# Kernel tuning notes

Hardware: AMD Instinct MI355X
Metric: run time of the kernel (lower is better)

Reference implementation:

```python
import jax, jax.numpy as jnp
import numpy as np

N_NODES = 100000
N_EDGES = 1600000
IN_DIM = 128
OUT_DIM = 64


def setup_inputs() -> dict:
    key = jax.random.key(0)
    k1, k2, k3, k4, k5 = jax.random.split(key, 5)
    X = jax.random.normal(k1, (N_NODES, IN_DIM), dtype=jnp.float32)
    # reset_parameters: uniform(-stdv, stdv), stdv = 1/sqrt(output_dim)
    stdv = 1.0 / np.sqrt(OUT_DIM)
    weights = jax.random.uniform(k2, (IN_DIM, OUT_DIM), dtype=jnp.float32,
                                 minval=-stdv, maxval=stdv)
    attention_w = jax.random.normal(k3, (1, 1), dtype=jnp.float32)
    edge_src = jnp.sort(jax.random.randint(k4, (N_EDGES,), 0, N_NODES, dtype=jnp.int32))
    edge_dst = jax.random.randint(k5, (N_EDGES,), 0, N_NODES, dtype=jnp.int32)
    return {"X": X, "weights": weights, "attention_w": attention_w,
            "edge_src": edge_src, "edge_dst": edge_dst}


def reference(X, weights, attention_w, edge_src, edge_dst):
    # Dense projection: X_prime = X @ W  -> [N, OUT_DIM]
    X_prime = X @ weights
    # forward_ef: per-edge scalar feature = <X_prime[src], X_prime[dst]>  -> [E]
    src_feat = X_prime[edge_src]          # [E, OUT_DIM] irregular gather
    dst_feat = X_prime[edge_dst]          # [E, OUT_DIM] irregular gather
    edge_feature = jnp.einsum('ed,ed->e', src_feat, dst_feat)
    # edge_attentions = edge_feature[:, None] @ attention_w -> [n_heads=1, E]
    att = edge_feature * attention_w[0, 0]            # [E]
    # forward_AGNN: out[i] = sum_{e:(i->j)} att[e] * X_prime[j]
    msgs = att[:, None] * dst_feat                    # [E, OUT_DIM]
    out = jax.ops.segment_sum(msgs, edge_src, num_segments=X.shape[0])
    return out
```

## Files before the change

### kernel.cpp

```cpp
#include <hip/hip_runtime.h>
#include <stdint.h>

#define N_NODES 100000
#define N_EDGES 1600000
#define IN_DIM 128
#define OUT_DIM 64

typedef __bf16 bf16x8 __attribute__((ext_vector_type(8)));
typedef float  f32x4  __attribute__((ext_vector_type(4)));

__device__ __forceinline__ uint16_t f2bf(float f) {
    uint32_t u = __float_as_uint(f);
    return (uint16_t)((u + 0x7fffu + ((u >> 16) & 1u)) >> 16);
}
__device__ __forceinline__ void unpack8(const uint4& v, float* x) {
    x[0] = __uint_as_float(v.x << 16); x[1] = __uint_as_float(v.x & 0xffff0000u);
    x[2] = __uint_as_float(v.y << 16); x[3] = __uint_as_float(v.y & 0xffff0000u);
    x[4] = __uint_as_float(v.z << 16); x[5] = __uint_as_float(v.z & 0xffff0000u);
    x[6] = __uint_as_float(v.w << 16); x[7] = __uint_as_float(v.w & 0xffff0000u);
}

__global__ __launch_bounds__(256) void prep(const int* __restrict__ src,
                                            const float* __restrict__ W,
                                            int* __restrict__ row_ptr,
                                            uint4* __restrict__ Wfrag) {
    const int b = blockIdx.x;
    if (b < N_EDGES / 256) {
        int e = b * 256 + threadIdx.x;
        int s = src[e];
        if (e == 0) {
            for (int i = 0; i <= s; ++i) row_ptr[i] = 0;
        } else {
            int sp = src[e - 1];
            for (int i = sp + 1; i <= s; ++i) row_ptr[i] = e;
        }
        if (e == N_EDGES - 1) {
            for (int i = s + 1; i <= N_NODES; ++i) row_ptr[i] = N_EDGES;
        }
    } else {
        int item = (b - N_EDGES / 256) * 256 + threadIdx.x;
        if (item < 1024) {
            int f = item >> 6, lane = item & 63;
            int ct = f >> 2, ks = f & 3;
            int col = ct * 16 + (lane & 15);
            int kb  = ks * 32 + (lane >> 4) * 8;
            uint32_t u[4];
            #pragma unroll
            for (int j = 0; j < 4; ++j) {
                uint32_t lo = f2bf(W[(kb + 2 * j)     * OUT_DIM + col]);
                uint32_t hi = f2bf(W[(kb + 2 * j + 1) * OUT_DIM + col]);
                u[j] = lo | (hi << 16);
            }
            Wfrag[f * 64 + lane] = make_uint4(u[0], u[1], u[2], u[3]);
        }
    }
}

__global__ __launch_bounds__(256) void gemm_xw(const float* __restrict__ X,
                                               const uint4* __restrict__ Wfrag,
                                               uint16_t* __restrict__ XPb,
                                               int nRows) {
    const int t = threadIdx.x;
    const int lane = t & 63;

    bf16x8 bfr[16];
    #pragma unroll
    for (int f = 0; f < 16; ++f)
        bfr[f] = __builtin_bit_cast(bf16x8, Wfrag[f * 64 + lane]);

    const int rowBase = blockIdx.x * 64 + (t >> 6) * 16;
    const int r  = rowBase + (lane & 15);
    const int kb = (lane >> 4) * 8;
    const bool inb = r < nRows;

    f32x4 acc[4] = {{0,0,0,0},{0,0,0,0},{0,0,0,0},{0,0,0,0}};

    #pragma unroll
    for (int ks = 0; ks < 4; ++ks) {
        float4 x0 = make_float4(0.f,0.f,0.f,0.f), x1 = x0;
        if (inb) {
            const float* p = &X[(size_t)r * IN_DIM + ks * 32 + kb];
            x0 = *(const float4*)&p[0];
            x1 = *(const float4*)&p[4];
        }
        bf16x8 a;
        a[0]=(__bf16)x0.x; a[1]=(__bf16)x0.y; a[2]=(__bf16)x0.z; a[3]=(__bf16)x0.w;
        a[4]=(__bf16)x1.x; a[5]=(__bf16)x1.y; a[6]=(__bf16)x1.z; a[7]=(__bf16)x1.w;
        #pragma unroll
        for (int ct = 0; ct < 4; ++ct)
            acc[ct] = __builtin_amdgcn_mfma_f32_16x16x32_bf16(a, bfr[ct * 4 + ks], acc[ct], 0, 0, 0);
    }

    const int orow = rowBase + (lane >> 4) * 4;
    const int ocol = lane & 15;
    #pragma unroll
    for (int ct = 0; ct < 4; ++ct) {
        #pragma unroll
        for (int rr = 0; rr < 4; ++rr) {
            int gr = orow + rr;
            if (gr < nRows) XPb[(size_t)gr * OUT_DIM + ct * 16 + ocol] = f2bf(acc[ct][rr]);
        }
    }
}

__global__ __launch_bounds__(256) void agnn_edge(const uint16_t* __restrict__ XPb,
                                                 const int* __restrict__ row_ptr,
                                                 const int* __restrict__ dst,
                                                 const float* __restrict__ aw,
                                                 float* __restrict__ out) {
    const int t = threadIdx.x;
    const int lane = t & 63;
    const int node = blockIdx.x * 4 + (t >> 6);
    if (node >= N_NODES) return;
    const int g = lane >> 3, sl = lane & 7;

    const int lo = row_ptr[node];
    const int hi = row_ptr[node + 1];

    float xq[8];
    {
        uint4 q = *(const uint4*)&XPb[(size_t)node * OUT_DIM + sl * 8];
        unpack8(q, xq);
    }
    float acc[8] = {0.f,0.f,0.f,0.f,0.f,0.f,0.f,0.f};

    for (int e0 = lo; e0 < hi; e0 += 16) {
        const int eA = e0 + g, eB = eA + 8;
        uint4 ra = make_uint4(0u,0u,0u,0u), rb = ra;
        if (eA < hi) {
            int d = dst[eA];
            ra = *(const uint4*)&XPb[(size_t)d * OUT_DIM + sl * 8];
        }
        if (eB < hi) {
            int d = dst[eB];
            rb = *(const uint4*)&XPb[(size_t)d * OUT_DIM + sl * 8];
        }
        float xd[8];
        unpack8(ra, xd);
        float p = xq[0] * xd[0];
        #pragma unroll
        for (int j = 1; j < 8; ++j) p = fmaf(xq[j], xd[j], p);
        p += __shfl_xor(p, 1); p += __shfl_xor(p, 2); p += __shfl_xor(p, 4);
        #pragma unroll
        for (int j = 0; j < 8; ++j) acc[j] = fmaf(p, xd[j], acc[j]);

        unpack8(rb, xd);
        float p2 = xq[0] * xd[0];
        #pragma unroll
        for (int j = 1; j < 8; ++j) p2 = fmaf(xq[j], xd[j], p2);
        p2 += __shfl_xor(p2, 1); p2 += __shfl_xor(p2, 2); p2 += __shfl_xor(p2, 4);
        #pragma unroll
        for (int j = 0; j < 8; ++j) acc[j] = fmaf(p2, xd[j], acc[j]);
    }

    #pragma unroll
    for (int m = 8; m <= 32; m <<= 1) {
        #pragma unroll
        for (int j = 0; j < 8; ++j) acc[j] += __shfl_xor(acc[j], m);
    }
    if (g == 0) {
        const float a = aw[0];
        float* o = &out[(size_t)node * OUT_DIM + sl * 8];
        *(float4*)&o[0] = make_float4(acc[0]*a, acc[1]*a, acc[2]*a, acc[3]*a);
        *(float4*)&o[4] = make_float4(acc[4]*a, acc[5]*a, acc[6]*a, acc[7]*a);
    }
}

extern "C" void kernel_launch(void* const* d_in, const int* in_sizes, int n_in,
                              void* d_out, int out_size, void* d_ws, size_t ws_size,
                              hipStream_t stream) {
    const float* X   = (const float*)d_in[0];
    const float* W   = (const float*)d_in[1];
    const float* aw  = (const float*)d_in[2];
    const int*   src = (const int*)d_in[3];
    const int*   dst = (const int*)d_in[4];
    float* out = (float*)d_out;

    uint16_t* XPb     = (uint16_t*)d_ws;
    int*      row_ptr = (int*)((char*)d_ws + (size_t)N_NODES * OUT_DIM * 2);
    uint4*    Wfrag   = (uint4*)((char*)d_ws + 13200016);

    prep<<<N_EDGES / 256 + 4, 256, 0, stream>>>(src, W, row_ptr, Wfrag);
    gemm_xw<<<(N_NODES + 63) / 64, 256, 0, stream>>>(X, Wfrag, XPb, N_NODES);
    agnn_edge<<<N_NODES / 4, 256, 0, stream>>>(XPb, row_ptr, dst, aw, out);
}
```

Baseline: 70.53 us.

## Store projected features as fp16 and use fdot2 with wider gather batches

Switches the intermediate projected-feature buffer from bf16 to fp16 so the per-edge dot product can use packed fdot2 instructions instead of unpacking to fp32 and doing scalar FMAs. The edge loop now processes 32 edges per iteration, issuing all four destination-index loads and then all four row gathers before computing, so more memory requests are in flight. It also adds a min-blocks hint to launch bounds. fp16 has a narrower range than bf16, which risks overflow if projected values grow large, though the test inputs keep them small.

```diff
diff --git a/kernel.cpp b/kernel.cpp
--- a/kernel.cpp
+++ b/kernel.cpp
@@ -6,18 +6,32 @@
 #define IN_DIM 128
 #define OUT_DIM 64
 
-typedef __bf16 bf16x8 __attribute__((ext_vector_type(8)));
-typedef float  f32x4  __attribute__((ext_vector_type(4)));
+typedef __bf16    bf16x8 __attribute__((ext_vector_type(8)));
+typedef float     f32x4  __attribute__((ext_vector_type(4)));
+typedef _Float16  h2     __attribute__((ext_vector_type(2)));
 
 __device__ __forceinline__ uint16_t f2bf(float f) {
     uint32_t u = __float_as_uint(f);
     return (uint16_t)((u + 0x7fffu + ((u >> 16) & 1u)) >> 16);
 }
-__device__ __forceinline__ void unpack8(const uint4& v, float* x) {
-    x[0] = __uint_as_float(v.x << 16); x[1] = __uint_as_float(v.x & 0xffff0000u);
-    x[2] = __uint_as_float(v.y << 16); x[3] = __uint_as_float(v.y & 0xffff0000u);
-    x[4] = __uint_as_float(v.z << 16); x[5] = __uint_as_float(v.z & 0xffff0000u);
-    x[6] = __uint_as_float(v.w << 16); x[7] = __uint_as_float(v.w & 0xffff0000u);
+__device__ __forceinline__ float hdot8(uint4 a, uint4 b, float c) {
+#if __has_builtin(__builtin_amdgcn_fdot2)
+    c = __builtin_amdgcn_fdot2(__builtin_bit_cast(h2, a.x), __builtin_bit_cast(h2, b.x), c, false);
+    c = __builtin_amdgcn_fdot2(__builtin_bit_cast(h2, a.y), __builtin_bit_cast(h2, b.y), c, false);
+    c = __builtin_amdgcn_fdot2(__builtin_bit_cast(h2, a.z), __builtin_bit_cast(h2, b.z), c, false);
+    c = __builtin_amdgcn_fdot2(__builtin_bit_cast(h2, a.w), __builtin_bit_cast(h2, b.w), c, false);
+#else
+    const h2 qa[4] = {__builtin_bit_cast(h2,a.x),__builtin_bit_cast(h2,a.y),
+                      __builtin_bit_cast(h2,a.z),__builtin_bit_cast(h2,a.w)};
+    const h2 qb[4] = {__builtin_bit_cast(h2,b.x),__builtin_bit_cast(h2,b.y),
+                      __builtin_bit_cast(h2,b.z),__builtin_bit_cast(h2,b.w)};
+    #pragma unroll
+    for (int i = 0; i < 4; ++i) {
+        c = fmaf((float)qa[i][0], (float)qb[i][0], c);
+        c = fmaf((float)qa[i][1], (float)qb[i][1], c);
+    }
+#endif
+    return c;
 }
 
 __global__ __launch_bounds__(256) void prep(const int* __restrict__ src,
@@ -58,7 +72,7 @@
 
 __global__ __launch_bounds__(256) void gemm_xw(const float* __restrict__ X,
                                                const uint4* __restrict__ Wfrag,
-                                               uint16_t* __restrict__ XPb,
+                                               _Float16* __restrict__ XPh,
                                                int nRows) {
     const int t = threadIdx.x;
     const int lane = t & 63;
@@ -98,59 +112,60 @@
         #pragma unroll
         for (int rr = 0; rr < 4; ++rr) {
             int gr = orow + rr;
-            if (gr < nRows) XPb[(size_t)gr * OUT_DIM + ct * 16 + ocol] = f2bf(acc[ct][rr]);
-        }
-    }
-}
-
-__global__ __launch_bounds__(256) void agnn_edge(const uint16_t* __restrict__ XPb,
-                                                 const int* __restrict__ row_ptr,
-                                                 const int* __restrict__ dst,
-                                                 const float* __restrict__ aw,
-                                                 float* __restrict__ out) {
+            if (gr < nRows) XPh[(size_t)gr * OUT_DIM + ct * 16 + ocol] = (_Float16)acc[ct][rr];
+        }
+    }
+}
+
+__global__ __launch_bounds__(256, 6) void agnn_edge(const _Float16* __restrict__ XPh,
+                                                    const int* __restrict__ row_ptr,
+                                                    const int* __restrict__ dst,
+                                                    const float* __restrict__ aw,
+                                                    float* __restrict__ out) {
     const int t = threadIdx.x;
     const int lane = t & 63;
     const int node = blockIdx.x * 4 + (t >> 6);
-    if (node >= N_NODES) return;
     const int g = lane >> 3, sl = lane & 7;
 
     const int lo = row_ptr[node];
     const int hi = row_ptr[node + 1];
 
-    float xq[8];
-    {
-        uint4 q = *(const uint4*)&XPb[(size_t)node * OUT_DIM + sl * 8];
-        unpack8(q, xq);
-    }
+    const uint4 q = *(const uint4*)&XPh[(size_t)node * OUT_DIM + sl * 8];
     float acc[8] = {0.f,0.f,0.f,0.f,0.f,0.f,0.f,0.f};
 
-    for (int e0 = lo; e0 < hi; e0 += 16) {
-        const int eA = e0 + g, eB = eA + 8;
-        uint4 ra = make_uint4(0u,0u,0u,0u), rb = ra;
-        if (eA < hi) {
-            int d = dst[eA];
-            ra = *(const uint4*)&XPb[(size_t)d * OUT_DIM + sl * 8];
-        }
-        if (eB < hi) {
-            int d = dst[eB];
-            rb = *(const uint4*)&XPb[(size_t)d * OUT_DIM + sl * 8];
-        }
-        float xd[8];
-        unpack8(ra, xd);
-        float p = xq[0] * xd[0];
-        #pragma unroll
-        for (int j = 1; j < 8; ++j) p = fmaf(xq[j], xd[j], p);
-        p += __shfl_xor(p, 1); p += __shfl_xor(p, 2); p += __shfl_xor(p, 4);
-        #pragma unroll
-        for (int j = 0; j < 8; ++j) acc[j] = fmaf(p, xd[j], acc[j]);
-
-        unpack8(rb, xd);
-        float p2 = xq[0] * xd[0];
-        #pragma unroll
-        for (int j = 1; j < 8; ++j) p2 = fmaf(xq[j], xd[j], p2);
-        p2 += __shfl_xor(p2, 1); p2 += __shfl_xor(p2, 2); p2 += __shfl_xor(p2, 4);
-        #pragma unroll
-        for (int j = 0; j < 8; ++j) acc[j] = fmaf(p2, xd[j], acc[j]);
+    for (int base = lo; base < hi; base += 32) {
+        int dx[4];
+        #pragma unroll
+        for (int c = 0; c < 4; ++c) {
+            int e = base + c * 8 + g;
+            dx[c] = (e < hi) ? dst[e] : -1;
+        }
+        uint4 xd[4];
+        #pragma unroll
+        for (int c = 0; c < 4; ++c) {
+            xd[c] = make_uint4(0u, 0u, 0u, 0u);
+            if (dx[c] >= 0)
+                xd[c] = *(const uint4*)&XPh[(size_t)dx[c] * OUT_DIM + sl * 8];
+        }
+        #pragma unroll
+        for (int c = 0; c < 4; ++c) {
+            float p = hdot8(q, xd[c], 0.f);
+            p += __shfl_xor(p, 1);
+            p += __shfl_xor(p, 2);
+            p += __shfl_xor(p, 4);
+            const h2 d0 = __builtin_bit_cast(h2, xd[c].x);
+            const h2 d1 = __builtin_bit_cast(h2, xd[c].y);
+            const h2 d2 = __builtin_bit_cast(h2, xd[c].z);
+            const h2 d3 = __builtin_bit_cast(h2, xd[c].w);
+            acc[0] = fmaf(p, (float)d0[0], acc[0]);
+            acc[1] = fmaf(p, (float)d0[1], acc[1]);
+            acc[2] = fmaf(p, (float)d1[0], acc[2]);
+            acc[3] = fmaf(p, (float)d1[1], acc[3]);
+            acc[4] = fmaf(p, (float)d2[0], acc[4]);
+            acc[5] = fmaf(p, (float)d2[1], acc[5]);
+            acc[6] = fmaf(p, (float)d3[0], acc[6]);
+            acc[7] = fmaf(p, (float)d3[1], acc[7]);
+        }
     }
 
     #pragma unroll
@@ -176,11 +191,11 @@
     const int*   dst = (const int*)d_in[4];
     float* out = (float*)d_out;
 
-    uint16_t* XPb     = (uint16_t*)d_ws;
+    _Float16* XPh     = (_Float16*)d_ws;
     int*      row_ptr = (int*)((char*)d_ws + (size_t)N_NODES * OUT_DIM * 2);
     uint4*    Wfrag   = (uint4*)((char*)d_ws + 13200016);
 
     prep<<<N_EDGES / 256 + 4, 256, 0, stream>>>(src, W, row_ptr, Wfrag);
-    gemm_xw<<<(N_NODES + 63) / 64, 256, 0, stream>>>(X, Wfrag, XPb, N_NODES);
-    agnn_edge<<<N_NODES / 4, 256, 0, stream>>>(XPb, row_ptr, dst, aw, out);
-}
+    gemm_xw<<<(N_NODES + 63) / 64, 256, 0, stream>>>(X, Wfrag, XPh, N_NODES);
+    agnn_edge<<<N_NODES / 4, 256, 0, stream>>>(XPh, row_ptr, dst, aw, out);
+}
```

After: 67.22 us. -4.7%, faster.
